# Performance work log

Hardware: AMD Instinct MI355X
Metric: run time of the kernel (lower is better)

The kernel has to match this reference:

```python
import jax, jax.numpy as jnp
import numpy as np

N, D, E, L = 50000, 128, 800000, 3


def setup_inputs() -> dict:
    key = jax.random.key(0)
    ks = jax.random.split(key, 4)
    scale = 1.0 / np.sqrt(D)
    x = jax.random.normal(ks[0], (N, D), dtype=jnp.float32)
    edge_index = jax.random.randint(ks[1], (2, E), 0, N, dtype=jnp.int64)
    W1 = jax.random.normal(ks[2], (L, D, D), dtype=jnp.float32) * scale
    W2 = jax.random.normal(ks[3], (L, D, D), dtype=jnp.float32) * scale
    b1 = jnp.zeros((L, D), dtype=jnp.float32)
    b2 = jnp.zeros((L, D), dtype=jnp.float32)
    return {"x": x, "edge_index": edge_index, "W1": W1, "b1": b1, "W2": W2, "b2": b2}


def reference(x, edge_index, W1, b1, W2, b2):
    # GIN: for each conv, agg_i = (1+eps)*x_i + sum_{(j->i)} x_j  (eps=0),
    # then h = nn(agg) with nn = Linear->ReLU->Linear, then outer ReLU.
    src = edge_index[0]
    dst = edge_index[1]
    n = x.shape[0]
    for l in range(W1.shape[0]):
        agg = x + jax.ops.segment_sum(x[src], dst, num_segments=n)  # [N, D]
        h = jnp.maximum(agg @ W1[l] + b1[l], 0.0)                   # inner ReLU
        x = jnp.maximum(h @ W2[l] + b2[l], 0.0)                     # outer ReLU
    return x
```

## Files before the change

### kernel.cpp

```cpp
#include <hip/hip_runtime.h>
#include <cstdint>


constexpr int N = 50000;
constexpr int D = 128;
constexpr int E = 800000;
constexpr int L = 3;
constexpr int WROW = 136;
constexpr int PSH = 9;
constexpr int PN = 1 << PSH;
constexpr int K = (N + PN - 1) >> PSH;
constexpr int SLACK = 7 * PN;
constexpr int ABLK = 2048;
constexpr int NAB = (E + ABLK - 1) / ABLK;

typedef _Float16 f16;
typedef _Float16 f16x8 __attribute__((ext_vector_type(8)));
typedef float f32x4 __attribute__((ext_vector_type(4)));

__device__ __forceinline__ bool ei_is64(const int* ei) {
  return (ei[1] == 0) && (ei[3] == 0) && (ei[5] == 0);
}
__device__ __forceinline__ int ei_src(const int* ei, int e, bool is64) {
  return is64 ? ei[2 * (size_t)e] : ei[e];
}
__device__ __forceinline__ int ei_dst(const int* ei, int e, bool is64) {
  return is64 ? ei[2 * ((size_t)E + e)] : ei[(size_t)E + e];
}

__global__ __launch_bounds__(256) void k_init(const float* __restrict__ x0,
                                              const int* __restrict__ ei,
                                              const float* __restrict__ W1,
                                              const float* __restrict__ W2,
                                              f16* __restrict__ Wt,
                                              f16* __restrict__ xh,
                                              int2* __restrict__ srcdst,
                                              int* __restrict__ gcnt) {
  __shared__ int hist[K];
  const int bid = blockIdx.x;
  if (bid < 384) {
    int i = bid * 256 + threadIdx.x;
    int m = i >> 14;
    int c = (i >> 7) & 127;
    int k = i & 127;
    const float* src = (m < L) ? (W1 + (size_t)m * D * D)
                               : (W2 + (size_t)(m - L) * D * D);
    Wt[i] = (f16)src[(size_t)k * D + c];
  } else if (bid < 384 + 3125) {
    int i = (bid - 384) * 256 + threadIdx.x;
    float4 v0 = *(const float4*)(x0 + (size_t)i * 8);
    float4 v1 = *(const float4*)(x0 + (size_t)i * 8 + 4);
    f16x8 o = {(f16)v0.x, (f16)v0.y, (f16)v0.z, (f16)v0.w,
               (f16)v1.x, (f16)v1.y, (f16)v1.z, (f16)v1.w};
    *(f16x8*)(xh + (size_t)i * 8) = o;
  } else if (bid < 384 + 3125 + NAB) {
    const int b = bid - (384 + 3125);
    for (int i = threadIdx.x; i < K; i += 256) hist[i] = 0;
    __syncthreads();
    const int base = b * ABLK;
    const int nHere = min(ABLK, E - base);
    bool is64 = ei_is64(ei);
#pragma unroll
    for (int r = 0; r < ABLK / 256; ++r) {
      int idx = r * 256 + threadIdx.x;
      if (idx < nHere) {
        int e = base + idx;
        int s = ei_src(ei, e, is64);
        int d = ei_dst(ei, e, is64);
        srcdst[e] = make_int2(s, d);
        atomicAdd(&hist[d >> PSH], 1);
      }
    }
    __syncthreads();
    for (int i = threadIdx.x; i < K; i += 256) gcnt[i * NAB + b] = hist[i];
  } else {
    if (threadIdx.x < 16)
      *(f16x8*)(xh + (size_t)N * D + threadIdx.x * 8) = (f16x8){};
  }
}

__global__ __launch_bounds__(256) void k_gbase(const int* __restrict__ gcnt,
                                               int* __restrict__ gbase,
                                               int* __restrict__ psize) {
  __shared__ int s[256];
  __shared__ int carry;
  const int p = blockIdx.x;
  const int tid = threadIdx.x;
  if (tid == 0) carry = 0;
  __syncthreads();
  for (int chunk = 0; chunk < 2; ++chunk) {
    int i = chunk * 256 + tid;
    int v = (i < NAB) ? gcnt[p * NAB + i] : 0;
    s[tid] = v;
    __syncthreads();
#pragma unroll
    for (int o = 1; o < 256; o <<= 1) {
      int t = (tid >= o) ? s[tid - o] : 0;
      __syncthreads();
      s[tid] += t;
      __syncthreads();
    }
    int excl = s[tid] - v + carry;
    if (i < NAB) gbase[p * NAB + i] = excl;
    __syncthreads();
    if (tid == 255) carry = carry + s[255];
    __syncthreads();
  }
  if (tid == 0) psize[p] = carry;
}

__device__ __forceinline__ void pscan_inblock(const int* __restrict__ psize,
                                              int* __restrict__ pb) {
  const int tid = threadIdx.x;
  if (tid < K) pb[tid] = psize[tid];
  __syncthreads();
  if (tid == 0) {
    int r = 0;
    for (int i = 0; i < K; ++i) {
      int v = pb[i];
      pb[i] = r;
      r += v;
    }
  }
  __syncthreads();
}

__global__ __launch_bounds__(256) void k_scat(const int2* __restrict__ srcdst,
                                              const int* __restrict__ gbase,
                                              const int* __restrict__ psize,
                                              int2* __restrict__ part) {
  __shared__ int rankc[K];
  __shared__ int pb[K];
  const int b = blockIdx.x;
  const int tid = threadIdx.x;
  for (int i = tid; i < K; i += 256) rankc[i] = 0;
  pscan_inblock(psize, pb);
  const int base = b * ABLK;
  const int nHere = min(ABLK, E - base);
#pragma unroll
  for (int r = 0; r < ABLK / 256; ++r) {
    int idx = r * 256 + tid;
    if (idx < nHere) {
      int2 sd = srcdst[base + idx];
      int p = sd.y >> PSH;
      int lr = atomicAdd(&rankc[p], 1);
      part[pb[p] + gbase[p * NAB + b] + lr] = sd;
    }
  }
}

__global__ __launch_bounds__(256) void k_fin(const int2* __restrict__ part,
                                             const int* __restrict__ psize,
                                             int2* __restrict__ offpe,
                                             int* __restrict__ ssrc,
                                             int* __restrict__ perm) {
  __shared__ int hist[PN];
  __shared__ int bbase[PN];
  __shared__ int rc[PN];
  __shared__ int s[256];
  __shared__ int pb[K];
  __shared__ int tbase[16];
  __shared__ int carry;
  const int p = blockIdx.x;
  const int tid = threadIdx.x;
  const int lo = p << PSH;
  const int nn = min(PN, N - lo);
  for (int i = tid; i < PN; i += 256) { hist[i] = 0; rc[i] = 0; }
  if (tid == 0) carry = 0;
  if (tid < 16) tbase[tid] = 0;
  pscan_inblock(psize, pb);
  const int ebeg = pb[p], eend = pb[p] + psize[p];
  const int padbase = pb[p] + p * SLACK;
  for (int e = ebeg + tid; e < eend; e += 256)
    atomicAdd(&hist[part[e].y - lo], 1);
  __syncthreads();
  for (int i = tid; i < nn; i += 256)
    atomicAdd(&tbase[min((hist[i] + 7) >> 3, 15)], 1);
  for (int chunk = 0; chunk < PN / 256; ++chunk) {
    int i = chunk * 256 + tid;
    int v = (hist[i] + 7) & ~7;
    s[tid] = v;
    __syncthreads();
#pragma unroll
    for (int o = 1; o < 256; o <<= 1) {
      int t = (tid >= o) ? s[tid - o] : 0;
      __syncthreads();
      s[tid] += t;
      __syncthreads();
    }
    bbase[i] = s[tid] - v + carry;
    __syncthreads();
    if (tid == 255) carry = carry + s[255];
    __syncthreads();
  }
  if (tid == 0) {
    int r = 0;
#pragma unroll
    for (int q = 0; q < 16; ++q) { int v = tbase[q]; tbase[q] = r; r += v; }
  }
  __syncthreads();
  for (int i = tid; i < nn; i += 256) {
    int st = padbase + bbase[i];
    int deg = hist[i];
    int pd = (deg + 7) & ~7;
    offpe[lo + i] = make_int2(st, st + pd);
    for (int j = deg; j < pd; ++j) ssrc[st + j] = N;
    int r = atomicAdd(&tbase[min((deg + 7) >> 3, 15)], 1);
    perm[lo + r] = lo + i;
  }
  __syncthreads();
  for (int e = ebeg + tid; e < eend; e += 256) {
    int2 sd = part[e];
    int b = sd.y - lo;
    int r = atomicAdd(&rc[b], 1);
    ssrc[padbase + bbase[b] + r] = sd.x;
  }
}

__global__ __launch_bounds__(256) void k_gather_f16(const f16* __restrict__ x,
                                                    const int2* __restrict__ offpe,
                                                    const int* __restrict__ ssrc,
                                                    const int* __restrict__ perm,
                                                    f16* __restrict__ agg) {
  const int slot = blockIdx.x * 16 + (threadIdx.x >> 4);
  const int n = perm[slot];
  const int d0 = (threadIdx.x & 15) << 3;
  f16x8 v = *(const f16x8*)(x + (size_t)n * D + d0);
  float acc[8];
#pragma unroll
  for (int j = 0; j < 8; ++j) acc[j] = (float)v[j];
  const int2 oe = offpe[n];
  for (int p = oe.x; p < oe.y; p += 8) {
    f16x8 u[8];
#pragma unroll
    for (int q = 0; q < 8; ++q) {
      int s = ssrc[p + q];
      u[q] = *(const f16x8*)(x + (size_t)s * D + d0);
    }
#pragma unroll
    for (int q = 0; q < 8; ++q)
#pragma unroll
      for (int j = 0; j < 8; ++j) acc[j] += (float)u[q][j];
  }
  f16x8 o;
#pragma unroll
  for (int j = 0; j < 8; ++j) o[j] = (f16)acc[j];
  *(f16x8*)(agg + (size_t)n * D + d0) = o;
}

__global__ __launch_bounds__(512) void k_gemm_fused(const f16* __restrict__ A,
                                                    const f16* __restrict__ Wt1,
                                                    const f16* __restrict__ Wt2,
                                                    const float* __restrict__ b1,
                                                    const float* __restrict__ b2,
                                                    f16* __restrict__ Ch,
                                                    float* __restrict__ Cf) {
  __shared__ f16 Ws[2][128 * WROW];
  {
    const f16x8* g1 = (const f16x8*)Wt1;
    const f16x8* g2 = (const f16x8*)Wt2;
    for (int i = threadIdx.x; i < 2048; i += 512) {
      int c = i >> 4;
      int k8 = (i & 15) << 3;
      *(f16x8*)&Ws[0][c * WROW + k8] = g1[i];
      *(f16x8*)&Ws[1][c * WROW + k8] = g2[i];
    }
  }

  const int w = threadIdx.x >> 6;
  const int l = threadIdx.x & 63;
  const int l15 = l & 15;
  const int g = l >> 4;
  const int r0 = blockIdx.x * 128 + w * 16;

  const int arow = min(r0 + l15, N - 1);
  const f16* Arow = A + (size_t)arow * D;
  f16x8 a[4];
#pragma unroll
  for (int t = 0; t < 4; ++t)
    a[t] = *(const f16x8*)(Arow + t * 32 + g * 8);

  float bc1[8], bc2[8];
#pragma unroll
  for (int c = 0; c < 8; ++c) {
    bc1[c] = b1[c * 16 + l15];
    bc2[c] = b2[c * 16 + l15];
  }
  __syncthreads();

  f32x4 acc[8];
#pragma unroll
  for (int c = 0; c < 8; ++c) acc[c] = (f32x4){0.f, 0.f, 0.f, 0.f};
#pragma unroll
  for (int t = 0; t < 4; ++t) {
#pragma unroll
    for (int c = 0; c < 8; ++c) {
      f16x8 b = *(const f16x8*)&Ws[0][(c * 16 + l15) * WROW + t * 32 + g * 8];
      acc[c] = __builtin_amdgcn_mfma_f32_16x16x32_f16(a[t], b, acc[c], 0, 0, 0);
    }
  }
  __syncthreads();

  f16* hbuf = &Ws[0][0];
#pragma unroll
  for (int r = 0; r < 4; ++r) {
    int hr = w * 16 + g * 4 + r;
#pragma unroll
    for (int c = 0; c < 8; ++c) {
      float vv = fmaxf(acc[c][r] + bc1[c], 0.0f);
      hbuf[hr * WROW + c * 16 + l15] = (f16)vv;
    }
  }
  __syncthreads();

  f16x8 a2[4];
#pragma unroll
  for (int t = 0; t < 4; ++t)
    a2[t] = *(const f16x8*)&hbuf[(w * 16 + l15) * WROW + t * 32 + g * 8];

#pragma unroll
  for (int c = 0; c < 8; ++c) acc[c] = (f32x4){0.f, 0.f, 0.f, 0.f};
#pragma unroll
  for (int t = 0; t < 4; ++t) {
#pragma unroll
    for (int c = 0; c < 8; ++c) {
      f16x8 b = *(const f16x8*)&Ws[1][(c * 16 + l15) * WROW + t * 32 + g * 8];
      acc[c] = __builtin_amdgcn_mfma_f32_16x16x32_f16(a2[t], b, acc[c], 0, 0, 0);
    }
  }

#pragma unroll
  for (int r = 0; r < 4; ++r) {
    int rr = r0 + g * 4 + r;
    if (rr < N) {
#pragma unroll
      for (int c = 0; c < 8; ++c) {
        int col = c * 16 + l15;
        float vv = fmaxf(acc[c][r] + bc2[c], 0.0f);
        if (Cf) Cf[(size_t)rr * D + col] = vv;
        else    Ch[(size_t)rr * D + col] = (f16)vv;
      }
    }
  }
}

extern "C" void kernel_launch(void* const* d_in, const int* in_sizes, int n_in,
                              void* d_out, int out_size, void* d_ws, size_t ws_size,
                              hipStream_t stream) {
  const float* x0 = (const float*)d_in[0];
  const int* ei   = (const int*)d_in[1];
  const float* W1 = (const float*)d_in[2];
  const float* b1 = (const float*)d_in[3];
  const float* W2 = (const float*)d_in[4];
  const float* b2 = (const float*)d_in[5];
  float* out = (float*)d_out;

  f16* xh      = (f16*)d_ws;
  f16* aggh    = xh + (size_t)(N + 1) * D;
  f16* Wt      = aggh + (size_t)N * D;
  int2* srcdst = (int2*)(Wt + (size_t)2 * L * D * D);
  int2* part   = srcdst + E;
  int2* offpe  = part + E;
  int* gcnt    = (int*)(offpe + N);
  int* gbase   = gcnt + (size_t)K * NAB;
  int* psize   = gbase + (size_t)K * NAB;
  int* perm    = psize + K;
  int* ssrc    = perm + N;

  const dim3 blk(256);

  k_init<<<384 + 3125 + NAB + 1, blk, 0, stream>>>(x0, ei, W1, W2, Wt, xh,
                                                   srcdst, gcnt);
  k_gbase<<<K, blk, 0, stream>>>(gcnt, gbase, psize);
  k_scat<<<NAB, blk, 0, stream>>>(srcdst, gbase, psize, part);
  k_fin<<<K, blk, 0, stream>>>(part, psize, offpe, ssrc, perm);

  const int gemm_blocks = (N + 127) / 128;
  const int gather_blocks = N / 16;

  for (int l = 0; l < L; ++l) {
    k_gather_f16<<<gather_blocks, blk, 0, stream>>>(xh, offpe, ssrc, perm, aggh);
    k_gemm_fused<<<gemm_blocks, dim3(512), 0, stream>>>(
        aggh, Wt + (size_t)l * D * D, Wt + (size_t)(L + l) * D * D,
        b1 + (size_t)l * D, b2 + (size_t)l * D, xh,
        (l == L - 1) ? out : nullptr);
  }
}
```

Measured before the change: 186.4 us.

## Drop gbase kernel and degree-sorted perm; vectorize gather index loads

Removes the separate k_gbase prefix-scan kernel: each scatter and finalize block instead recomputes partition totals and its own per-block offsets by serially summing rows of the count matrix. Drops the degree-bucket permutation so the gather walks nodes in natural order, and aligns padded segment starts to 8 so source indices can be read as two int4 loads. It also adds an occupancy hint to the gather. This saves one launch and a perm indirection, but each of the ~391 scatter blocks now performs redundant K×NAB serial reads of gcnt. Losing degree-sorted scheduling may also increase warp imbalance in the gather.

```diff
diff --git a/kernel.cpp b/kernel.cpp
--- a/kernel.cpp
+++ b/kernel.cpp
@@ -10,7 +10,7 @@
 constexpr int PSH = 9;
 constexpr int PN = 1 << PSH;
 constexpr int K = (N + PN - 1) >> PSH;
-constexpr int SLACK = 7 * PN;
+constexpr int SLACK = 7 * PN + 8;
 constexpr int ABLK = 2048;
 constexpr int NAB = (E + ABLK - 1) / ABLK;
 
@@ -79,40 +79,22 @@
   }
 }
 
-__global__ __launch_bounds__(256) void k_gbase(const int* __restrict__ gcnt,
-                                               int* __restrict__ gbase,
-                                               int* __restrict__ psize) {
-  __shared__ int s[256];
-  __shared__ int carry;
-  const int p = blockIdx.x;
+__device__ __forceinline__ void bases_inblock(const int* __restrict__ gcnt,
+                                              int upto_b,
+                                              int* __restrict__ pb,
+                                              int* __restrict__ own) {
   const int tid = threadIdx.x;
-  if (tid == 0) carry = 0;
-  __syncthreads();
-  for (int chunk = 0; chunk < 2; ++chunk) {
-    int i = chunk * 256 + tid;
-    int v = (i < NAB) ? gcnt[p * NAB + i] : 0;
-    s[tid] = v;
-    __syncthreads();
-#pragma unroll
-    for (int o = 1; o < 256; o <<= 1) {
-      int t = (tid >= o) ? s[tid - o] : 0;
-      __syncthreads();
-      s[tid] += t;
-      __syncthreads();
-    }
-    int excl = s[tid] - v + carry;
-    if (i < NAB) gbase[p * NAB + i] = excl;
-    __syncthreads();
-    if (tid == 255) carry = carry + s[255];
-    __syncthreads();
-  }
-  if (tid == 0) psize[p] = carry;
-}
-
-__device__ __forceinline__ void pscan_inblock(const int* __restrict__ psize,
-                                              int* __restrict__ pb) {
-  const int tid = threadIdx.x;
-  if (tid < K) pb[tid] = psize[tid];
+  if (tid < K) {
+    int tot = 0, ow = 0;
+    const int* row = gcnt + tid * NAB;
+    for (int i = 0; i < NAB; ++i) {
+      int v = row[i];
+      tot += v;
+      if (i < upto_b) ow += v;
+    }
+    pb[tid] = tot;
+    if (own) own[tid] = ow;
+  }
   __syncthreads();
   if (tid == 0) {
     int r = 0;
@@ -126,15 +108,15 @@
 }
 
 __global__ __launch_bounds__(256) void k_scat(const int2* __restrict__ srcdst,
-                                              const int* __restrict__ gbase,
-                                              const int* __restrict__ psize,
+                                              const int* __restrict__ gcnt,
                                               int2* __restrict__ part) {
   __shared__ int rankc[K];
   __shared__ int pb[K];
+  __shared__ int own[K];
   const int b = blockIdx.x;
   const int tid = threadIdx.x;
   for (int i = tid; i < K; i += 256) rankc[i] = 0;
-  pscan_inblock(psize, pb);
+  bases_inblock(gcnt, b, pb, own);
   const int base = b * ABLK;
   const int nHere = min(ABLK, E - base);
 #pragma unroll
@@ -144,22 +126,21 @@
       int2 sd = srcdst[base + idx];
       int p = sd.y >> PSH;
       int lr = atomicAdd(&rankc[p], 1);
-      part[pb[p] + gbase[p * NAB + b] + lr] = sd;
+      part[pb[p] + own[p] + lr] = sd;
     }
   }
 }
 
 __global__ __launch_bounds__(256) void k_fin(const int2* __restrict__ part,
-                                             const int* __restrict__ psize,
+                                             const int* __restrict__ gcnt,
                                              int2* __restrict__ offpe,
-                                             int* __restrict__ ssrc,
-                                             int* __restrict__ perm) {
+                                             int* __restrict__ ssrc) {
   __shared__ int hist[PN];
   __shared__ int bbase[PN];
   __shared__ int rc[PN];
   __shared__ int s[256];
   __shared__ int pb[K];
-  __shared__ int tbase[16];
+  __shared__ int psz[K];
   __shared__ int carry;
   const int p = blockIdx.x;
   const int tid = threadIdx.x;
@@ -167,15 +148,18 @@
   const int nn = min(PN, N - lo);
   for (int i = tid; i < PN; i += 256) { hist[i] = 0; rc[i] = 0; }
   if (tid == 0) carry = 0;
-  if (tid < 16) tbase[tid] = 0;
-  pscan_inblock(psize, pb);
-  const int ebeg = pb[p], eend = pb[p] + psize[p];
-  const int padbase = pb[p] + p * SLACK;
+  if (tid < K) {
+    int tot = 0;
+    const int* row = gcnt + tid * NAB;
+    for (int i = 0; i < NAB; ++i) tot += row[i];
+    psz[tid] = tot;
+  }
+  bases_inblock(gcnt, -1, pb, nullptr);
+  const int ebeg = pb[p], eend = pb[p] + psz[p];
+  const int padbase = ((pb[p] + 7) & ~7) + p * SLACK;
   for (int e = ebeg + tid; e < eend; e += 256)
     atomicAdd(&hist[part[e].y - lo], 1);
   __syncthreads();
-  for (int i = tid; i < nn; i += 256)
-    atomicAdd(&tbase[min((hist[i] + 7) >> 3, 15)], 1);
   for (int chunk = 0; chunk < PN / 256; ++chunk) {
     int i = chunk * 256 + tid;
     int v = (hist[i] + 7) & ~7;
@@ -193,20 +177,12 @@
     if (tid == 255) carry = carry + s[255];
     __syncthreads();
   }
-  if (tid == 0) {
-    int r = 0;
-#pragma unroll
-    for (int q = 0; q < 16; ++q) { int v = tbase[q]; tbase[q] = r; r += v; }
-  }
-  __syncthreads();
   for (int i = tid; i < nn; i += 256) {
     int st = padbase + bbase[i];
     int deg = hist[i];
     int pd = (deg + 7) & ~7;
     offpe[lo + i] = make_int2(st, st + pd);
     for (int j = deg; j < pd; ++j) ssrc[st + j] = N;
-    int r = atomicAdd(&tbase[min((deg + 7) >> 3, 15)], 1);
-    perm[lo + r] = lo + i;
   }
   __syncthreads();
   for (int e = ebeg + tid; e < eend; e += 256) {
@@ -217,13 +193,11 @@
   }
 }
 
-__global__ __launch_bounds__(256) void k_gather_f16(const f16* __restrict__ x,
-                                                    const int2* __restrict__ offpe,
-                                                    const int* __restrict__ ssrc,
-                                                    const int* __restrict__ perm,
-                                                    f16* __restrict__ agg) {
-  const int slot = blockIdx.x * 16 + (threadIdx.x >> 4);
-  const int n = perm[slot];
+__global__ __launch_bounds__(256, 4) void k_gather_f16(const f16* __restrict__ x,
+                                                       const int2* __restrict__ offpe,
+                                                       const int* __restrict__ ssrc,
+                                                       f16* __restrict__ agg) {
+  const int n = blockIdx.x * 16 + (threadIdx.x >> 4);
   const int d0 = (threadIdx.x & 15) << 3;
   f16x8 v = *(const f16x8*)(x + (size_t)n * D + d0);
   float acc[8];
@@ -231,16 +205,20 @@
   for (int j = 0; j < 8; ++j) acc[j] = (float)v[j];
   const int2 oe = offpe[n];
   for (int p = oe.x; p < oe.y; p += 8) {
-    f16x8 u[8];
-#pragma unroll
-    for (int q = 0; q < 8; ++q) {
-      int s = ssrc[p + q];
-      u[q] = *(const f16x8*)(x + (size_t)s * D + d0);
-    }
-#pragma unroll
-    for (int q = 0; q < 8; ++q)
-#pragma unroll
-      for (int j = 0; j < 8; ++j) acc[j] += (float)u[q][j];
+    int4 sa = *(const int4*)(ssrc + p);
+    int4 sb = *(const int4*)(ssrc + p + 4);
+    f16x8 u0 = *(const f16x8*)(x + (size_t)sa.x * D + d0);
+    f16x8 u1 = *(const f16x8*)(x + (size_t)sa.y * D + d0);
+    f16x8 u2 = *(const f16x8*)(x + (size_t)sa.z * D + d0);
+    f16x8 u3 = *(const f16x8*)(x + (size_t)sa.w * D + d0);
+    f16x8 u4 = *(const f16x8*)(x + (size_t)sb.x * D + d0);
+    f16x8 u5 = *(const f16x8*)(x + (size_t)sb.y * D + d0);
+    f16x8 u6 = *(const f16x8*)(x + (size_t)sb.z * D + d0);
+    f16x8 u7 = *(const f16x8*)(x + (size_t)sb.w * D + d0);
+#pragma unroll
+    for (int j = 0; j < 8; ++j)
+      acc[j] += (float)u0[j] + (float)u1[j] + (float)u2[j] + (float)u3[j] +
+                (float)u4[j] + (float)u5[j] + (float)u6[j] + (float)u7[j];
   }
   f16x8 o;
 #pragma unroll
@@ -362,24 +340,20 @@
   int2* part   = srcdst + E;
   int2* offpe  = part + E;
   int* gcnt    = (int*)(offpe + N);
-  int* gbase   = gcnt + (size_t)K * NAB;
-  int* psize   = gbase + (size_t)K * NAB;
-  int* perm    = psize + K;
-  int* ssrc    = perm + N;
+  int* ssrc    = gcnt + (size_t)K * NAB;
 
   const dim3 blk(256);
 
   k_init<<<384 + 3125 + NAB + 1, blk, 0, stream>>>(x0, ei, W1, W2, Wt, xh,
                                                    srcdst, gcnt);
-  k_gbase<<<K, blk, 0, stream>>>(gcnt, gbase, psize);
-  k_scat<<<NAB, blk, 0, stream>>>(srcdst, gbase, psize, part);
-  k_fin<<<K, blk, 0, stream>>>(part, psize, offpe, ssrc, perm);
+  k_scat<<<NAB, blk, 0, stream>>>(srcdst, gcnt, part);
+  k_fin<<<K, blk, 0, stream>>>(part, gcnt, offpe, ssrc);
 
   const int gemm_blocks = (N + 127) / 128;
   const int gather_blocks = N / 16;
 
   for (int l = 0; l < L; ++l) {
-    k_gather_f16<<<gather_blocks, blk, 0, stream>>>(xh, offpe, ssrc, perm, aggh);
+    k_gather_f16<<<gather_blocks, blk, 0, stream>>>(xh, offpe, ssrc, aggh);
     k_gemm_fused<<<gemm_blocks, dim3(512), 0, stream>>>(
         aggh, Wt + (size_t)l * D * D, Wt + (size_t)(L + l) * D * D,
         b1 + (size_t)l * D, b2 + (size_t)l * D, xh,
```

Result: no change. 189.4 us (+1.6%).
